# Kernel tuning notes

Measured on AMD Instinct MI355X. Metric: run time of the kernel, lower is better.

## Reference

```python
import jax, jax.numpy as jnp
import numpy as np

N = 50000
E = 1600000
IN_DIM = 128
HEADS = 4
OUT_DIM = 32
NEG_SLOPE = 0.2


def setup_inputs() -> dict:
    key = jax.random.key(0)
    k1, k2, k3, k4, k5, k6 = jax.random.split(key, 6)
    x = jax.random.normal(k1, (N, IN_DIM), dtype=jnp.float32)
    src = jax.random.randint(k2, (E,), 0, N)
    dst = jax.random.randint(k3, (E,), 0, N)
    edge_index = jnp.stack([src, dst], axis=0).astype(jnp.int64)
    W = jax.random.normal(k4, (IN_DIM, HEADS * OUT_DIM), dtype=jnp.float32) * 0.08
    att = jax.random.normal(k5, (HEADS, 2 * OUT_DIM), dtype=jnp.float32) * 0.1
    bias = jnp.zeros((HEADS * OUT_DIM,), dtype=jnp.float32)
    return {"x": x, "edge_index": edge_index, "W": W, "att": att, "bias": bias}


def reference(x, edge_index, W, att, bias):
    src, dst = edge_index[0], edge_index[1]
    n = x.shape[0]
    # Linear projection -> [N, H, F]
    Wh = (x @ W).reshape(n, HEADS, OUT_DIM)
    # Per-node attention score halves (equivalent to (cat[Wh_i,Wh_j]*att).sum(-1))
    a_src = jnp.einsum("nhf,hf->nh", Wh, att[:, :OUT_DIM])  # [N, H]
    a_dst = jnp.einsum("nhf,hf->nh", Wh, att[:, OUT_DIM:])  # [N, H]
    logits = jax.nn.leaky_relu(a_src[src] + a_dst[dst], negative_slope=NEG_SLOPE)  # [E, H]
    # Segment softmax over destination nodes (numerically stable)
    seg_max = jax.ops.segment_max(logits, dst, num_segments=n)  # [N, H]
    exp_s = jnp.exp(logits - seg_max[dst])
    denom = jnp.clip(jax.ops.segment_sum(exp_s, dst, num_segments=n), 1e-9, None)
    alpha = exp_s / denom[dst]  # [E, H]
    # Weighted messages from SOURCE features, scatter-sum to destinations
    messages = alpha[:, :, None] * Wh[src]  # [E, H, F]
    out = jax.ops.segment_sum(messages.reshape(-1, HEADS * OUT_DIM), dst, num_segments=n)
    return out + bias
```

## Files before the change

### kernel.cpp

```cpp
#include <hip/hip_runtime.h>
#include <hip/hip_fp16.h>
#include <math.h>

#define N_NODES 50000
#define E_EDGES 1600000
#define IN_DIM 128
#define HEADS 4
#define OUT_DIM 32
#define HF 128
#define NEG_SLOPE 0.2f
#define NBUCK 196
#define BCAP 8800

__global__ __launch_bounds__(256) void gat_proj(
        const float* __restrict__ x, const float* __restrict__ W,
        const float* __restrict__ att, __half* __restrict__ Whh,
        float* __restrict__ a_src, float* __restrict__ a_dst) {
    __shared__ float Ws[64][HF];
    __shared__ float xs[64][132];
    __shared__ float atts[HEADS][2 * OUT_DIM];

    const int tid = threadIdx.x;
    if (tid < 64) ((float4*)&atts[0][0])[tid] = ((const float4*)att)[tid];

    const int rowBase = blockIdx.x * 64;
    const int rowsHere = min(64, N_NODES - rowBase);
    const float4* x4 = (const float4*)(x + (size_t)rowBase * IN_DIM);
    for (int i = tid; i < rowsHere * 32; i += 256) {
        const int r = i >> 5, q = i & 31;
        *(float4*)&xs[r][q * 4] = x4[i];
    }

    const int rg = tid >> 4;
    const int cg = tid & 15;
    const int r0 = rg * 4;
    const int c0 = cg * 8;
    const int h  = cg >> 2;
    const int f0 = (cg & 3) * 8;

    float acc[4][8];
#pragma unroll
    for (int i = 0; i < 4; ++i)
#pragma unroll
        for (int j = 0; j < 8; ++j) acc[i][j] = 0.f;

    float4* Ws4 = (float4*)&Ws[0][0];
#pragma unroll
    for (int half = 0; half < 2; ++half) {
        __syncthreads();
        const float4* Wsrc = (const float4*)(W + half * 64 * HF);
#pragma unroll
        for (int i = 0; i < 8; ++i) Ws4[tid + 256 * i] = Wsrc[tid + 256 * i];
        __syncthreads();

        const int kb = half * 64;
        for (int k0 = 0; k0 < 64; k0 += 4) {
            float4 a4[4];
#pragma unroll
            for (int i = 0; i < 4; ++i)
                a4[i] = *(const float4*)&xs[r0 + i][kb + k0];
#pragma unroll
            for (int kk = 0; kk < 4; ++kk) {
                float4 w0 = *(const float4*)&Ws[k0 + kk][c0];
                float4 w1 = *(const float4*)&Ws[k0 + kk][c0 + 4];
                const float wv[8] = {w0.x, w0.y, w0.z, w0.w,
                                     w1.x, w1.y, w1.z, w1.w};
                const float av[4] = {(&a4[0].x)[kk], (&a4[1].x)[kk],
                                     (&a4[2].x)[kk], (&a4[3].x)[kk]};
#pragma unroll
                for (int j = 0; j < 8; ++j) {
                    acc[0][j] = fmaf(av[0], wv[j], acc[0][j]);
                    acc[1][j] = fmaf(av[1], wv[j], acc[1][j]);
                    acc[2][j] = fmaf(av[2], wv[j], acc[2][j]);
                    acc[3][j] = fmaf(av[3], wv[j], acc[3][j]);
                }
            }
        }
    }

#pragma unroll
    for (int i = 0; i < 4; ++i) {
        const int r = r0 + i;
        if (r >= rowsHere) break;
        const int row = rowBase + r;
        union { __half2 h[4]; float4 f; } u;
        u.h[0] = __floats2half2_rn(acc[i][0], acc[i][1]);
        u.h[1] = __floats2half2_rn(acc[i][2], acc[i][3]);
        u.h[2] = __floats2half2_rn(acc[i][4], acc[i][5]);
        u.h[3] = __floats2half2_rn(acc[i][6], acc[i][7]);
        *(float4*)(Whh + (size_t)row * HF + c0) = u.f;

        float ps = 0.f, pd = 0.f;
#pragma unroll
        for (int j = 0; j < 8; ++j) {
            ps = fmaf(acc[i][j], atts[h][f0 + j], ps);
            pd = fmaf(acc[i][j], atts[h][OUT_DIM + f0 + j], pd);
        }
        ps += __shfl_xor(ps, 1, 64); ps += __shfl_xor(ps, 2, 64);
        pd += __shfl_xor(pd, 1, 64); pd += __shfl_xor(pd, 2, 64);
        if ((cg & 3) == 0) {
            a_src[row * HEADS + h] = ps;
            a_dst[row * HEADS + h] = pd;
        }
    }
}

__global__ __launch_bounds__(256) void gat_p1(
        const int* __restrict__ ei, int* __restrict__ gCount,
        unsigned int* __restrict__ gBuck) {
    __shared__ int hist[NBUCK];
    __shared__ int cur[NBUCK];
    const int t = threadIdx.x;
    for (int i = t; i < NBUCK; i += 256) hist[i] = 0;
    __syncthreads();

    unsigned int keys[16];
    bool valid[4];
    const int base4 = blockIdx.x * 1024 + t;
#pragma unroll
    for (int j = 0; j < 4; ++j) {
        const int i4 = base4 + 256 * j;
        valid[j] = (i4 < E_EDGES / 4);
        if (valid[j]) {
            const int4 s4 = ((const int4*)ei)[i4];
            const int4 d4 = ((const int4*)(ei + E_EDGES))[i4];
            keys[j * 4 + 0] = ((unsigned)d4.x << 16) | (unsigned)s4.x;
            keys[j * 4 + 1] = ((unsigned)d4.y << 16) | (unsigned)s4.y;
            keys[j * 4 + 2] = ((unsigned)d4.z << 16) | (unsigned)s4.z;
            keys[j * 4 + 3] = ((unsigned)d4.w << 16) | (unsigned)s4.w;
#pragma unroll
            for (int q = 0; q < 4; ++q)
                atomicAdd(&hist[keys[j * 4 + q] >> 24], 1);
        }
    }
    __syncthreads();
    for (int i = t; i < NBUCK; i += 256)
        cur[i] = atomicAdd(&gCount[i], hist[i]);
    __syncthreads();
#pragma unroll
    for (int j = 0; j < 4; ++j) {
        if (!valid[j]) continue;
#pragma unroll
        for (int q = 0; q < 4; ++q) {
            const unsigned int k = keys[j * 4 + q];
            const int b = k >> 24;
            const int p = atomicAdd(&cur[b], 1);
            if (p < BCAP) gBuck[(size_t)b * BCAP + p] = k;
        }
    }
}

__global__ __launch_bounds__(256) void gat_p2(
        const int* __restrict__ gCount, const unsigned int* __restrict__ gBuck,
        unsigned short* __restrict__ csr, int* __restrict__ offsets) {
    __shared__ int pre[256];
    __shared__ int hist[256];
    __shared__ int loc[256];
    __shared__ unsigned short out16[BCAP];
    const int b = blockIdx.x;
    const int t = threadIdx.x;

    int v = (t < NBUCK) ? min(gCount[t], BCAP) : 0;
    pre[t] = v;
    __syncthreads();
#pragma unroll
    for (int d = 1; d < 256; d <<= 1) {
        int u = (t >= d) ? pre[t - d] : 0;
        __syncthreads();
        pre[t] += u;
        __syncthreads();
    }
    const int total = pre[255];
    const int baseb = (b > 0) ? pre[b - 1] : 0;
    const int cnt = min(gCount[b], BCAP);

    hist[t] = 0;
    __syncthreads();
    for (int i = t; i < cnt; i += 256)
        atomicAdd(&hist[(gBuck[(size_t)b * BCAP + i] >> 16) & 255], 1);
    __syncthreads();
    const int hv = hist[t];
    loc[t] = hv;
    __syncthreads();
#pragma unroll
    for (int d = 1; d < 256; d <<= 1) {
        int u = (t >= d) ? loc[t - d] : 0;
        __syncthreads();
        loc[t] += u;
        __syncthreads();
    }
    const int myloc = loc[t] - hv;
    const int node = b * 256 + t;
    if (node < N_NODES) offsets[node] = baseb + myloc;
    if (b == 0 && t == 0) offsets[N_NODES] = total;
    __syncthreads();

    hist[t] = myloc;
    __syncthreads();
    for (int i = t; i < cnt; i += 256) {
        const unsigned int k = gBuck[(size_t)b * BCAP + i];
        const int n = (k >> 16) & 255;
        const int r = atomicAdd(&hist[n], 1);
        out16[r] = (unsigned short)(k & 0xFFFFu);
    }
    __syncthreads();
    for (int i = t; i < cnt; i += 256)
        csr[baseb + i] = out16[i];
}

__global__ __launch_bounds__(256) void gat_gather(
        const int* __restrict__ offsets, const unsigned short* __restrict__ csr,
        const float* __restrict__ a_src, const float* __restrict__ a_dst,
        const __half* __restrict__ Whh, const float* __restrict__ bias,
        float* __restrict__ out) {
    const int node = blockIdx.x * 4 + (threadIdx.x >> 6);
    const int lane = threadIdx.x & 63;
    if (node >= N_NODES) return;
    const int h = lane >> 4;
    const int hbase = lane & 48;
    const int sub = lane & 15;
    const float ad = a_dst[node * HEADS + h];
    const __half2* __restrict__ Wh2 = (const __half2*)Whh;

    float accx = 0.f, accy = 0.f, denOwn = 0.f;
    const int beg = offsets[node];
    const int cnt = offsets[node + 1] - beg;

    for (int base = 0; base < cnt; base += 64) {
        const int rem = min(64, cnt - base);
        const int idx = (base + lane < cnt) ? (int)csr[beg + base + lane] : 0;
        const int nchunk = (rem + 15) >> 4;
        for (int cj = 0; cj < nchunk; ++cj) {
            const int e0 = cj << 4;
            const int sOwn = __shfl(idx, e0 + sub, 64);
            float t = a_src[sOwn * 4 + h] + ad;
            t = fmaxf(t, NEG_SLOPE * t);
            float wOwn = __expf(t);
            if (base + e0 + sub >= cnt) wOwn = 0.f;
            denOwn += wOwn;

            const int jmax = min(16, rem - e0);
            int j = 0;
            for (; j + 4 <= jmax; j += 4) {
                const int s0 = __shfl(idx, e0 + j,     64);
                const int s1 = __shfl(idx, e0 + j + 1, 64);
                const int s2 = __shfl(idx, e0 + j + 2, 64);
                const int s3 = __shfl(idx, e0 + j + 3, 64);
                const __half2 v0 = Wh2[(size_t)s0 * 64 + lane];
                const __half2 v1 = Wh2[(size_t)s1 * 64 + lane];
                const __half2 v2 = Wh2[(size_t)s2 * 64 + lane];
                const __half2 v3 = Wh2[(size_t)s3 * 64 + lane];
                const float w0 = __shfl(wOwn, hbase + j,     64);
                const float w1 = __shfl(wOwn, hbase + j + 1, 64);
                const float w2 = __shfl(wOwn, hbase + j + 2, 64);
                const float w3 = __shfl(wOwn, hbase + j + 3, 64);
                const float2 f0 = __half22float2(v0);
                const float2 f1 = __half22float2(v1);
                const float2 f2 = __half22float2(v2);
                const float2 f3 = __half22float2(v3);
                accx = fmaf(w0, f0.x, accx); accy = fmaf(w0, f0.y, accy);
                accx = fmaf(w1, f1.x, accx); accy = fmaf(w1, f1.y, accy);
                accx = fmaf(w2, f2.x, accx); accy = fmaf(w2, f2.y, accy);
                accx = fmaf(w3, f3.x, accx); accy = fmaf(w3, f3.y, accy);
            }
            for (; j < jmax; ++j) {
                const int s = __shfl(idx, e0 + j, 64);
                const float w = __shfl(wOwn, hbase + j, 64);
                const float2 v = __half22float2(Wh2[(size_t)s * 64 + lane]);
                accx = fmaf(w, v.x, accx);
                accy = fmaf(w, v.y, accy);
            }
        }
    }
    float den = denOwn;
    den += __shfl_xor(den, 1, 64);
    den += __shfl_xor(den, 2, 64);
    den += __shfl_xor(den, 4, 64);
    den += __shfl_xor(den, 8, 64);

    const float inv = 1.f / fmaxf(den, 1e-9f);
    const float2 b2 = ((const float2*)bias)[lane];
    float2 o = {accx * inv + b2.x, accy * inv + b2.y};
    ((float2*)out)[(size_t)node * 64 + lane] = o;
}

extern "C" void kernel_launch(void* const* d_in, const int* in_sizes, int n_in,
                              void* d_out, int out_size, void* d_ws, size_t ws_size,
                              hipStream_t stream) {
    const float* x    = (const float*)d_in[0];
    const int*   ei   = (const int*)d_in[1];
    const float* W    = (const float*)d_in[2];
    const float* att  = (const float*)d_in[3];
    const float* bias = (const float*)d_in[4];
    float* out = (float*)d_out;

    __half* Whh   = (__half*)d_ws;
    float* a_src  = (float*)(Whh + (size_t)N_NODES * HF);
    float* a_dst  = a_src + (size_t)N_NODES * HEADS;
    unsigned int* gBuck = (unsigned int*)(a_dst + (size_t)N_NODES * HEADS);
    unsigned short* csr = (unsigned short*)(gBuck + (size_t)NBUCK * BCAP);
    int*   offsets = (int*)(csr + (size_t)E_EDGES);
    int*   gCount  = offsets + N_NODES + 8;

    hipMemsetAsync(gCount, 0, NBUCK * sizeof(int), stream);
    gat_proj<<<(N_NODES + 63) / 64, 256, 0, stream>>>(x, W, att, Whh, a_src, a_dst);
    gat_p1<<<(E_EDGES / 4 + 1023) / 1024, 256, 0, stream>>>(ei, gCount, gBuck);
    gat_p2<<<NBUCK, 256, 0, stream>>>(gCount, gBuck, csr, offsets);
    gat_gather<<<(N_NODES + 3) / 4, 256, 0, stream>>>(offsets, csr, a_src,
                                                      a_dst, Whh, bias, out);
}
```

Baseline: 210.0 us.

## Use fp16 MFMA for projection and batch 16 gathers per chunk

The projection GEMM moves from fp32 FMA on CUDA-core-style lanes to fp16 MFMA 16x16x32 instructions. A new small kernel transposes W to fp16, and a per-block fragment layout is staged in shared memory. Separately, the gather loop now issues all 16 source-row loads before consuming them, which raises memory-level parallelism. This adds an extra launch, and converting inputs to fp16 costs some precision.

```diff
diff --git a/kernel.cpp b/kernel.cpp
--- a/kernel.cpp
+++ b/kernel.cpp
@@ -12,95 +12,101 @@
 #define NBUCK 196
 #define BCAP 8800
 
+typedef _Float16 half8 __attribute__((ext_vector_type(8)));
+typedef float float4v __attribute__((ext_vector_type(4)));
+
+__global__ __launch_bounds__(256) void gat_wt(
+        const float* __restrict__ W, _Float16* __restrict__ Wt) {
+    const int n = blockIdx.x * 2 + (threadIdx.x >> 7);
+    const int k = threadIdx.x & 127;
+    Wt[n * 128 + k] = (_Float16)W[k * 128 + n];
+}
+
 __global__ __launch_bounds__(256) void gat_proj(
-        const float* __restrict__ x, const float* __restrict__ W,
+        const float* __restrict__ x, const _Float16* __restrict__ Wt,
         const float* __restrict__ att, __half* __restrict__ Whh,
         float* __restrict__ a_src, float* __restrict__ a_dst) {
-    __shared__ float Ws[64][HF];
-    __shared__ float xs[64][132];
-    __shared__ float atts[HEADS][2 * OUT_DIM];
-
-    const int tid = threadIdx.x;
-    if (tid < 64) ((float4*)&atts[0][0])[tid] = ((const float4*)att)[tid];
-
-    const int rowBase = blockIdx.x * 64;
+    __shared__ _Float16 xsh[64][136];
+    __shared__ float4 wfrag[2048 / 4 * 8 / 8];
+    __shared__ float atts[256];
+
+    const int tid  = threadIdx.x;
+    const int lane = tid & 63;
+    const int wv   = tid >> 6;
+    const int l15  = lane & 15;
+    const int quad = lane >> 4;
+
+    if (tid < 64) ((float4*)atts)[tid] = ((const float4*)att)[tid];
+
+    const int rowBase  = blockIdx.x * 64;
     const int rowsHere = min(64, N_NODES - rowBase);
+
     const float4* x4 = (const float4*)(x + (size_t)rowBase * IN_DIM);
     for (int i = tid; i < rowsHere * 32; i += 256) {
         const int r = i >> 5, q = i & 31;
-        *(float4*)&xs[r][q * 4] = x4[i];
-    }
-
-    const int rg = tid >> 4;
-    const int cg = tid & 15;
-    const int r0 = rg * 4;
-    const int c0 = cg * 8;
-    const int h  = cg >> 2;
-    const int f0 = (cg & 3) * 8;
-
-    float acc[4][8];
-#pragma unroll
-    for (int i = 0; i < 4; ++i)
-#pragma unroll
-        for (int j = 0; j < 8; ++j) acc[i][j] = 0.f;
-
-    float4* Ws4 = (float4*)&Ws[0][0];
-#pragma unroll
-    for (int half = 0; half < 2; ++half) {
-        __syncthreads();
-        const float4* Wsrc = (const float4*)(W + half * 64 * HF);
-#pragma unroll
-        for (int i = 0; i < 8; ++i) Ws4[tid + 256 * i] = Wsrc[tid + 256 * i];
-        __syncthreads();
-
-        const int kb = half * 64;
-        for (int k0 = 0; k0 < 64; k0 += 4) {
-            float4 a4[4];
-#pragma unroll
-            for (int i = 0; i < 4; ++i)
-                a4[i] = *(const float4*)&xs[r0 + i][kb + k0];
-#pragma unroll
-            for (int kk = 0; kk < 4; ++kk) {
-                float4 w0 = *(const float4*)&Ws[k0 + kk][c0];
-                float4 w1 = *(const float4*)&Ws[k0 + kk][c0 + 4];
-                const float wv[8] = {w0.x, w0.y, w0.z, w0.w,
-                                     w1.x, w1.y, w1.z, w1.w};
-                const float av[4] = {(&a4[0].x)[kk], (&a4[1].x)[kk],
-                                     (&a4[2].x)[kk], (&a4[3].x)[kk]};
-#pragma unroll
-                for (int j = 0; j < 8; ++j) {
-                    acc[0][j] = fmaf(av[0], wv[j], acc[0][j]);
-                    acc[1][j] = fmaf(av[1], wv[j], acc[1][j]);
-                    acc[2][j] = fmaf(av[2], wv[j], acc[2][j]);
-                    acc[3][j] = fmaf(av[3], wv[j], acc[3][j]);
-                }
+        float4 v = x4[i];
+        _Float16* p = &xsh[r][q * 4];
+        p[0] = (_Float16)v.x; p[1] = (_Float16)v.y;
+        p[2] = (_Float16)v.z; p[3] = (_Float16)v.w;
+    }
+
+    __shared__ float4 wf[32 * 64];
+    for (int i = tid; i < 32 * 64; i += 256) {
+        const int ln = i & 63, c = i >> 6;
+        const int s = c >> 3, t = c & 7;
+        const int n = t * 16 + (ln & 15);
+        const int k = s * 32 + (ln >> 4) * 8;
+        wf[i] = *(const float4*)(Wt + n * 128 + k);
+    }
+    __syncthreads();
+
+    float4v acc[8] = {};
+    half8 afr[4];
+#pragma unroll
+    for (int s = 0; s < 4; ++s)
+        afr[s] = *(const half8*)&xsh[wv * 16 + l15][s * 32 + quad * 8];
+#pragma unroll
+    for (int s = 0; s < 4; ++s) {
+#pragma unroll
+        for (int t = 0; t < 8; ++t) {
+            half8 b = *(const half8*)&wf[(s * 8 + t) * 64 + lane];
+            acc[t] = __builtin_amdgcn_mfma_f32_16x16x32_f16(afr[s], b, acc[t], 0, 0, 0);
+        }
+    }
+
+    float ps[4][4] = {}, pd[4][4] = {};
+#pragma unroll
+    for (int t = 0; t < 8; ++t) {
+        const int g = t >> 1;
+        const int f = ((t & 1) << 4) + l15;
+        const float as_ = atts[g * 64 + f];
+        const float ad_ = atts[g * 64 + 32 + f];
+#pragma unroll
+        for (int reg = 0; reg < 4; ++reg) {
+            ps[reg][g] = fmaf(acc[t][reg], as_, ps[reg][g]);
+            pd[reg][g] = fmaf(acc[t][reg], ad_, pd[reg][g]);
+        }
+    }
+#pragma unroll
+    for (int reg = 0; reg < 4; ++reg) {
+        const int rloc = wv * 16 + quad * 4 + reg;
+        const int row = rowBase + rloc;
+        if (rloc < rowsHere) {
+#pragma unroll
+            for (int t = 0; t < 8; ++t)
+                Whh[(size_t)row * HF + t * 16 + l15] = __float2half(acc[t][reg]);
+        }
+#pragma unroll
+        for (int g = 0; g < 4; ++g) {
+#pragma unroll
+            for (int d = 1; d < 16; d <<= 1) {
+                ps[reg][g] += __shfl_xor(ps[reg][g], d, 64);
+                pd[reg][g] += __shfl_xor(pd[reg][g], d, 64);
             }
         }
-    }
-
-#pragma unroll
-    for (int i = 0; i < 4; ++i) {
-        const int r = r0 + i;
-        if (r >= rowsHere) break;
-        const int row = rowBase + r;
-        union { __half2 h[4]; float4 f; } u;
-        u.h[0] = __floats2half2_rn(acc[i][0], acc[i][1]);
-        u.h[1] = __floats2half2_rn(acc[i][2], acc[i][3]);
-        u.h[2] = __floats2half2_rn(acc[i][4], acc[i][5]);
-        u.h[3] = __floats2half2_rn(acc[i][6], acc[i][7]);
-        *(float4*)(Whh + (size_t)row * HF + c0) = u.f;
-
-        float ps = 0.f, pd = 0.f;
-#pragma unroll
-        for (int j = 0; j < 8; ++j) {
-            ps = fmaf(acc[i][j], atts[h][f0 + j], ps);
-            pd = fmaf(acc[i][j], atts[h][OUT_DIM + f0 + j], pd);
-        }
-        ps += __shfl_xor(ps, 1, 64); ps += __shfl_xor(ps, 2, 64);
-        pd += __shfl_xor(pd, 1, 64); pd += __shfl_xor(pd, 2, 64);
-        if ((cg & 3) == 0) {
-            a_src[row * HEADS + h] = ps;
-            a_dst[row * HEADS + h] = pd;
+        if (rloc < rowsHere && l15 < 4) {
+            a_src[row * HEADS + l15] = ps[reg][l15];
+            a_dst[row * HEADS + l15] = pd[reg][l15];
         }
     }
 }
@@ -240,35 +246,31 @@
             denOwn += wOwn;
 
             const int jmax = min(16, rem - e0);
-            int j = 0;
-            for (; j + 4 <= jmax; j += 4) {
-                const int s0 = __shfl(idx, e0 + j,     64);
-                const int s1 = __shfl(idx, e0 + j + 1, 64);
-                const int s2 = __shfl(idx, e0 + j + 2, 64);
-                const int s3 = __shfl(idx, e0 + j + 3, 64);
-                const __half2 v0 = Wh2[(size_t)s0 * 64 + lane];
-                const __half2 v1 = Wh2[(size_t)s1 * 64 + lane];
-                const __half2 v2 = Wh2[(size_t)s2 * 64 + lane];
-                const __half2 v3 = Wh2[(size_t)s3 * 64 + lane];
-                const float w0 = __shfl(wOwn, hbase + j,     64);
-                const float w1 = __shfl(wOwn, hbase + j + 1, 64);
-                const float w2 = __shfl(wOwn, hbase + j + 2, 64);
-                const float w3 = __shfl(wOwn, hbase + j + 3, 64);
-                const float2 f0 = __half22float2(v0);
-                const float2 f1 = __half22float2(v1);
-                const float2 f2 = __half22float2(v2);
-                const float2 f3 = __half22float2(v3);
-                accx = fmaf(w0, f0.x, accx); accy = fmaf(w0, f0.y, accy);
-                accx = fmaf(w1, f1.x, accx); accy = fmaf(w1, f1.y, accy);
-                accx = fmaf(w2, f2.x, accx); accy = fmaf(w2, f2.y, accy);
-                accx = fmaf(w3, f3.x, accx); accy = fmaf(w3, f3.y, accy);
-            }
-            for (; j < jmax; ++j) {
-                const int s = __shfl(idx, e0 + j, 64);
-                const float w = __shfl(wOwn, hbase + j, 64);
-                const float2 v = __half22float2(Wh2[(size_t)s * 64 + lane]);
-                accx = fmaf(w, v.x, accx);
-                accy = fmaf(w, v.y, accy);
+            if (jmax == 16) {
+                int ss[16];
+#pragma unroll
+                for (int j = 0; j < 16; ++j) ss[j] = __shfl(idx, e0 + j, 64);
+                __half2 vv[16];
+#pragma unroll
+                for (int j = 0; j < 16; ++j)
+                    vv[j] = Wh2[(size_t)ss[j] * 64 + lane];
+                float ww[16];
+#pragma unroll
+                for (int j = 0; j < 16; ++j) ww[j] = __shfl(wOwn, hbase + j, 64);
+#pragma unroll
+                for (int j = 0; j < 16; ++j) {
+                    const float2 f = __half22float2(vv[j]);
+                    accx = fmaf(ww[j], f.x, accx);
+                    accy = fmaf(ww[j], f.y, accy);
+                }
+            } else {
+                for (int j = 0; j < jmax; ++j) {
+                    const int s = __shfl(idx, e0 + j, 64);
+                    const float w = __shfl(wOwn, hbase + j, 64);
+                    const float2 v = __half22float2(Wh2[(size_t)s * 64 + lane]);
+                    accx = fmaf(w, v.x, accx);
+                    accy = fmaf(w, v.y, accy);
+                }
             }
         }
     }
@@ -301,9 +303,11 @@
     unsigned short* csr = (unsigned short*)(gBuck + (size_t)NBUCK * BCAP);
     int*   offsets = (int*)(csr + (size_t)E_EDGES);
     int*   gCount  = offsets + N_NODES + 8;
+    _Float16* Wt   = (_Float16*)(gCount + 256);
 
     hipMemsetAsync(gCount, 0, NBUCK * sizeof(int), stream);
-    gat_proj<<<(N_NODES + 63) / 64, 256, 0, stream>>>(x, W, att, Whh, a_src, a_dst);
+    gat_wt<<<64, 256, 0, stream>>>(W, Wt);
+    gat_proj<<<(N_NODES + 63) / 64, 256, 0, stream>>>(x, Wt, att, Whh, a_src, a_dst);
     gat_p1<<<(E_EDGES / 4 + 1023) / 1024, 256, 0, stream>>>(ei, gCount, gBuck);
     gat_p2<<<NBUCK, 256, 0, stream>>>(gCount, gBuck, csr, offsets);
     gat_gather<<<(N_NODES + 3) / 4, 256, 0, stream>>>(offsets, csr, a_src,
```

New measurement: 211.2 us. No clear change (+0.6%).
